# Performance work log

Hardware: AMD Instinct MI355X
Metric: run time of the kernel (lower is better)

The kernel has to match this reference:

```python
import jax, jax.numpy as jnp
import numpy as np

B, T, D, H = 512, 64, 16, 1024  # H must equal T*D (required by the original reshape)


def setup_inputs() -> dict:
    key = jax.random.key(0)
    ks = list(jax.random.split(key, 30))
    def nrm(k, shape, s=0.05):
        return jax.random.normal(k, shape, dtype=jnp.float32) * s
    inp = {}
    inp["values"] = jax.random.normal(ks[0], (B, T, D), dtype=jnp.float32)
    inp["masks"] = (jax.random.uniform(ks[1], (B, T, D)) < 0.8).astype(jnp.float32)
    i = 2
    for pre in ("fw", "bw"):
        for l, din in ((0, D), (1, H)):
            inp[f"{pre}_Wih{l}"] = nrm(ks[i], (4 * H, din)); i += 1
            inp[f"{pre}_Whh{l}"] = nrm(ks[i], (4 * H, H)); i += 1
            inp[f"{pre}_bih{l}"] = nrm(ks[i], (4 * H,)); i += 1
            inp[f"{pre}_bhh{l}"] = nrm(ks[i], (4 * H,)); i += 1
    inp["out_W"] = nrm(ks[i], (D, H)); i += 1
    inp["out_b"] = nrm(ks[i], (D,)); i += 1
    inp["fcb_W"] = nrm(ks[i], (D, 1)); i += 1
    inp["fcb_b"] = nrm(ks[i], (D,)); i += 1
    inp["fce_W"] = nrm(ks[i], (D, 1)); i += 1
    inp["fce_b"] = nrm(ks[i], (D,)); i += 1
    return inp


def _lstm_cell(x, h, c, Wih, Whh, bih, bhh):
    # PyTorch LSTMCell: gate order i, f, g, o
    gates = x @ Wih.T + bih + h @ Whh.T + bhh
    i, f, g, o = jnp.split(gates, 4, axis=-1)
    c2 = jax.nn.sigmoid(f) * c + jax.nn.sigmoid(i) * jnp.tanh(g)
    return jax.nn.sigmoid(o) * jnp.tanh(c2), c2


def _forward(values, masks, fw_Wih0, fw_Whh0, fw_bih0, fw_bhh0, fw_Wih1, fw_Whh1, fw_bih1, fw_bhh1,
             bw_Wih0, bw_Whh0, bw_bih0, bw_bhh0, bw_Wih1, bw_Whh1, bw_bih1, bw_bhh1,
             out_W, out_b, fcb_W, fcb_b, fce_W, fce_b):
    Bc, Tc, Dc = values.shape
    zeros = jnp.zeros((Bc, H), values.dtype)
    bwd_values = jnp.flip(values, 1)
    bwd_masks = jnp.flip(masks, 1)
    # fc_begin/fc_end outputs are dead code in the original (init loop starts at layer 1)
    # Original pre-loop: layers 1..L-1 run once with zero inputs/states.
    hf1, cf1 = _lstm_cell(zeros, zeros, zeros, fw_Wih1, fw_Whh1, fw_bih1, fw_bhh1)
    hb1, cb1 = _lstm_cell(zeros, zeros, zeros, bw_Wih1, bw_Whh1, bw_bih1, bw_bhh1)
    carry0 = (zeros, zeros, hf1, cf1, zeros, zeros, hb1, cb1)

    def step(carry, xs):
        hf0, cf0, hf1, cf1, hb0, cb0, hb1, cb1 = carry
        x_f, m_f, x_b, m_b = xs
        cc_f = (1.0 - m_f) * (hf1 @ out_W.T + out_b) + m_f * x_f
        cc_b = (1.0 - m_b) * (hb1 @ out_W.T + out_b) + m_b * x_b
        hf0, cf0 = _lstm_cell(cc_f, hf0, cf0, fw_Wih0, fw_Whh0, fw_bih0, fw_bhh0)
        hf1, cf1 = _lstm_cell(hf0, hf1, cf1, fw_Wih1, fw_Whh1, fw_bih1, fw_bhh1)
        hb0, cb0 = _lstm_cell(cc_b, hb0, cb0, bw_Wih0, bw_Whh0, bw_bih0, bw_bhh0)
        hb1, cb1 = _lstm_cell(hb0, hb1, cb1, bw_Wih1, bw_Whh1, bw_bih1, bw_bhh1)
        return (hf0, cf0, hf1, cf1, hb0, cb0, hb1, cb1), None

    xs = (jnp.swapaxes(values, 0, 1), jnp.swapaxes(masks, 0, 1),
          jnp.swapaxes(bwd_values, 0, 1), jnp.swapaxes(bwd_masks, 0, 1))
    carry, _ = jax.lax.scan(step, carry0, xs)
    hf1, hb1 = carry[2], carry[6]
    # Original averages fwd with hidden-dim-flipped bwd hidden state
    h = (hf1 + jnp.flip(hb1, 1)) * 0.5
    imputations = h.reshape(Bc, Tc, Dc)
    imputed = imputations * (1.0 - masks) + values * masks
    return h, imputations, imputed


def reference(values, masks, fw_Wih0, fw_Whh0, fw_bih0, fw_bhh0, fw_Wih1, fw_Whh1, fw_bih1, fw_bhh1,
              bw_Wih0, bw_Whh0, bw_bih0, bw_bhh0, bw_Wih1, bw_Whh1, bw_bih1, bw_bhh1,
              out_W, out_b, fcb_W, fcb_b, fce_W, fce_b):
    return _forward(values, masks, fw_Wih0, fw_Whh0, fw_bih0, fw_bhh0, fw_Wih1, fw_Whh1, fw_bih1, fw_bhh1,
                    bw_Wih0, bw_Whh0, bw_bih0, bw_bhh0, bw_Wih1, bw_Whh1, bw_bih1, bw_bhh1,
                    out_W, out_b, fcb_W, fcb_b, fce_W, fce_b)
```

## Files before the change

### kernel.cpp

```cpp
#include <hip/hip_runtime.h>
#include <cstdint>
#include <cstddef>

typedef unsigned short u16;
typedef __attribute__((ext_vector_type(8))) short short8;
typedef __attribute__((ext_vector_type(4))) short short4v;
typedef __attribute__((ext_vector_type(4))) float f32x4;

#define NB 512
#define NT 64
#define ND 16
#define NH 1024
#define LDSBUF 12288

__device__ __forceinline__ u16 f2bf(float x) {
  union { float f; unsigned u; } v; v.f = x;
  unsigned r = v.u + 0x7fffu + ((v.u >> 16) & 1u);
  return (u16)(r >> 16);
}
__device__ __forceinline__ float bf2f(u16 u) {
  union { float f; unsigned u; } v; v.u = ((unsigned)u) << 16;
  return v.f;
}
__device__ __forceinline__ float sigf(float x) { return 1.f / (1.f + __expf(-x)); }

__device__ __forceinline__ void glds16(const void* g, void* l) {
  __builtin_amdgcn_global_load_lds((const __attribute__((address_space(1))) void*)g,
                                   (__attribute__((address_space(3))) void*)l, 16, 0, 0);
}

__device__ __forceinline__ int swz(int row, int col) {
  return ((((col >> 3) ^ (row & 7)) << 3) | (col & 7));
}

__device__ __forceinline__ int inv_np(int np) {
  int hb = np >> 6, g = (np >> 4) & 3, hlo = np & 15;
  return g * 1024 + hb * 16 + hlo;
}

__global__ void k_prep_big(const float* s0, const float* s1, const float* s2,
                           const float* s3, const float* s4, const float* s5, u16* dst) {
  for (unsigned q = blockIdx.x * 256 + threadIdx.x; q < (6u << 20); q += gridDim.x * 256) {
    int mat = q >> 20;
    int rem = q & ((1 << 20) - 1);
    int np = rem >> 8;
    int k = (rem & 255) * 4;
    int row = inv_np(np);
    const float* s = mat == 0 ? s0 : mat == 1 ? s1 : mat == 2 ? s2 : mat == 3 ? s3 : mat == 4 ? s4 : s5;
    float4 v = *(const float4*)(s + (size_t)row * NH + k);
    u16* d = dst + (size_t)mat * 4194304 + (size_t)np * NH + swz(np, k);
    d[0] = f2bf(v.x); d[1] = f2bf(v.y); d[2] = f2bf(v.z); d[3] = f2bf(v.w);
  }
}

__global__ void k_prep_small(const float* fwih0, const float* bwih0,
                             const float* fbi0, const float* fbh0, const float* fbi1, const float* fbh1,
                             const float* bbi0, const float* bbh0, const float* bbi1, const float* bbh1,
                             const float* outW,
                             u16* wih0p, float* biasb, u16* owbf) {
  int idx = blockIdx.x * 256 + threadIdx.x;
  if (idx < 524288) {
    int dir = idx >> 18;
    int r = idx & 262143;
    int np = r >> 6, d = r & 63;
    int row = inv_np(np);
    const float* s = dir ? bwih0 : fwih0;
    float v = (d < 16) ? s[row * 16 + d] : 0.f;
    wih0p[(size_t)dir * 262144 + (size_t)np * 64 + swz(np, d)] = f2bf(v);
  } else if (idx < 524288 + 16384) {
    int j = idx - 524288;
    int which = j >> 12;
    int np = j & 4095;
    int row = inv_np(np);
    const float* bi = which == 0 ? fbi0 : which == 1 ? fbi1 : which == 2 ? bbi0 : bbi1;
    const float* bh = which == 0 ? fbh0 : which == 1 ? fbh1 : which == 2 ? bbh0 : bbh1;
    biasb[which * 4096 + np] = bi[row] + bh[row];
  } else if (idx < 524288 + 16384 + 16384) {
    int j = idx - 524288 - 16384;
    owbf[j] = f2bf(outW[j]);
  }
}

__global__ void k_init(const float* fbi1, const float* fbh1, const float* bbi1, const float* bbh1,
                       float* c0, float* c1, u16* h0bf, u16* h1bf) {
  int idx = blockIdx.x * 256 + threadIdx.x;
  int dir = idx >> 19;
  int rem = idx & ((1 << 19) - 1);
  int b = rem >> 10, h = rem & 1023;
  const float* bi = dir ? bbi1 : fbi1;
  const float* bh = dir ? bbh1 : fbh1;
  float gi = bi[h] + bh[h];
  float gg = bi[2048 + h] + bh[2048 + h];
  float go = bi[3072 + h] + bh[3072 + h];
  float c = sigf(gi) * tanhf(gg);
  float hv = sigf(go) * tanhf(c);
  size_t o = (size_t)dir * 524288 + rem;
  c1[o] = c;
  h1bf[(size_t)(dir * 2) * 524288 + (size_t)b * NH + swz(b, h)] = f2bf(hv);
  c0[o] = 0.f;
  h0bf[(size_t)(dir * 2) * 524288 + rem] = 0;
}

__global__ __launch_bounds__(256) void k_cc0(const u16* h1f, const u16* h1b,
                                             const float* outW, float* partial) {
  int dir = blockIdx.y;
  int w = threadIdx.x >> 6, lane = threadIdx.x & 63;
  int b = blockIdx.x * 4 + w;
  const u16* hb = dir ? h1b : h1f;
  int key = b & 7;
  short8 ha = *(const short8*)(hb + (size_t)b * NH + ((lane * 2) ^ key) * 8);
  short8 hc = *(const short8*)(hb + (size_t)b * NH + ((lane * 2 + 1) ^ key) * 8);
  float hf[16];
#pragma unroll
  for (int j = 0; j < 8; ++j) { hf[j] = bf2f((u16)ha[j]); hf[8 + j] = bf2f((u16)hc[j]); }
  float sums[16];
#pragma unroll
  for (int d = 0; d < 16; ++d) {
    const float* wr = outW + (size_t)d * NH + lane * 16;
    float s = 0.f;
#pragma unroll
    for (int j = 0; j < 16; ++j) s += hf[j] * wr[j];
#pragma unroll
    for (int off = 32; off; off >>= 1) s += __shfl_xor(s, off);
    sums[d] = s;
  }
  if (lane == 0) {
    float* dst = partial + (size_t)dir * 524288 + (size_t)b * 16;
#pragma unroll
    for (int d = 0; d < 16; ++d) dst[d] = sums[d];
  }
}

struct StepCtx {
  u16* h0bf; u16* h1bf;
  const u16* wbig; const u16* wih0p;
  const float* biasb;
  float* c0; float* c1;
  float* partial;
  const float* values; const float* masks; const float* outb;
  const u16* owbf;
};

__device__ __forceinline__ void phase_g0(u16* SM, const StepCtx& a, int dir,
                                         int m_blk, int n_blk, int t, int p) {
  const int m0 = m_blk * 64, n0 = n_blk * 128;
  const int tid = threadIdx.x, w = tid >> 6, lane = tid & 63;
  const int srow = lane >> 3, scol = (lane & 7) * 8;
  const int wm = w >> 1, wn = w & 1;
  const int fr = lane & 15, fq = lane >> 4;
  const int key = fr & 7;
  const u16* h0_in = a.h0bf + (size_t)(dir * 2 + p) * 524288;
  u16* h0_out = a.h0bf + (size_t)(dir * 2 + 1 - p) * 524288;
  const u16* W00 = a.wbig + (size_t)(dir * 3 + 0) * 4194304;
  const u16* Wcc = a.wih0p + (size_t)dir * 262144;
  const float* bias0 = a.biasb + (size_t)dir * 2 * 4096;
  float* cs0 = a.c0 + (size_t)dir * 524288;

  int aoff[2][2], boff[4][2];
#pragma unroll
  for (int mi = 0; mi < 2; ++mi)
#pragma unroll
    for (int kk = 0; kk < 2; ++kk)
      aoff[mi][kk] = (wm * 32 + mi * 16 + fr) * 64 + ((fq + kk * 4) ^ key) * 8;
#pragma unroll
  for (int ni = 0; ni < 4; ++ni)
#pragma unroll
    for (int kk = 0; kk < 2; ++kk)
      boff[ni][kk] = 4096 + (wn * 64 + ni * 16 + fr) * 64 + ((fq + kk * 4) ^ key) * 8;

  f32x4 acc[2][4];
#pragma unroll
  for (int i = 0; i < 2; ++i)
#pragma unroll
    for (int j = 0; j < 4; ++j) acc[i][j] = f32x4{0.f, 0.f, 0.f, 0.f};

  {
    const int rl = tid >> 2, q = tid & 3;
    const int grow = m0 + rl;
    const int d4 = q * 4;
    float4 ps = {0.f, 0.f, 0.f, 0.f};
    const float* pp = a.partial + (size_t)dir * 524288 + (size_t)grow * 16 + d4;
    for (int nb = 0; nb < 64; ++nb) {
      float4 v = *(const float4*)(pp + (size_t)nb * 8192);
      ps.x += v.x; ps.y += v.y; ps.z += v.z; ps.w += v.w;
    }
    int tt = dir ? (NT - 1 - t) : t;
    float4 x = *(const float4*)(a.values + ((size_t)grow * NT + tt) * ND + d4);
    float4 m = *(const float4*)(a.masks + ((size_t)grow * NT + tt) * ND + d4);
    float4 ob = *(const float4*)(a.outb + d4);
    short4v cc;
    cc[0] = (short)f2bf((1.f - m.x) * (ps.x + ob.x) + m.x * x.x);
    cc[1] = (short)f2bf((1.f - m.y) * (ps.y + ob.y) + m.y * x.y);
    cc[2] = (short)f2bf((1.f - m.z) * (ps.z + ob.z) + m.z * x.z);
    cc[3] = (short)f2bf((1.f - m.w) * (ps.w + ob.w) + m.w * x.w);
    int k2 = rl & 7;
    *(short4v*)(SM + rl * 64 + (((d4 >> 3) ^ k2) << 3) + (d4 & 7)) = cc;
    short8 z8 = {0, 0, 0, 0, 0, 0, 0, 0};
    *(short8*)(SM + rl * 64 + (((2 + q) ^ k2) << 3)) = z8;
    if (q < 2) *(short8*)(SM + rl * 64 + (((6 + q) ^ k2) << 3)) = z8;
    asm volatile("s_waitcnt lgkmcnt(0)" ::: "memory");
    __builtin_amdgcn_sched_barrier(0);
  }

  auto stage0 = [&](int c) {
    int buf = c; while (buf >= 3) buf -= 3;
    u16* lb = SM + buf * LDSBUF;
    if (c == 0) {
#pragma unroll
      for (int k = 0; k < 4; ++k)
        glds16(Wcc + (size_t)(n0 + w * 32 + k * 8 + srow) * 64 + scol,
               lb + 4096 + (w * 32 + k * 8) * 64);
      return;
    }
    int ci = c - 1;
    const u16* pa = h0_in + (size_t)ci * 64;
    const u16* pw = W00 + (size_t)ci * 64;
    glds16(pa + (size_t)(m0 + w * 16 + srow) * NH + scol, lb + (w * 16) * 64);
    glds16(pa + (size_t)(m0 + w * 16 + 8 + srow) * NH + scol, lb + (w * 16 + 8) * 64);
#pragma unroll
    for (int k = 0; k < 4; ++k)
      glds16(pw + (size_t)(n0 + w * 32 + k * 8 + srow) * NH + scol,
             lb + 4096 + (w * 32 + k * 8) * 64);
  };

  stage0(0); stage0(1);
  for (int c = 0; c < 17; ++c) {
    if (c == 16) asm volatile("s_waitcnt vmcnt(0)" ::: "memory");
    else         asm volatile("s_waitcnt vmcnt(6)" ::: "memory");
    __builtin_amdgcn_s_barrier();
    __builtin_amdgcn_sched_barrier(0);
    if (c + 2 < 17) stage0(c + 2);
    int buf = c; while (buf >= 3) buf -= 3;
    const u16* base = SM + buf * LDSBUF;
    short8 af[2][2], bb[4][2];
#pragma unroll
    for (int kk = 0; kk < 2; ++kk) {
#pragma unroll
      for (int mi = 0; mi < 2; ++mi) af[mi][kk] = *(const short8*)(base + aoff[mi][kk]);
#pragma unroll
      for (int ni = 0; ni < 4; ++ni) bb[ni][kk] = *(const short8*)(base + boff[ni][kk]);
    }
#pragma unroll
    for (int kk = 0; kk < 2; ++kk)
#pragma unroll
      for (int mi = 0; mi < 2; ++mi)
#pragma unroll
        for (int ni = 0; ni < 4; ++ni)
          acc[mi][ni] = __builtin_amdgcn_mfma_f32_16x16x32_bf16(af[mi][kk], bb[ni][kk], acc[mi][ni], 0, 0, 0);
  }

  const int hg = ((n0 + wn * 64) >> 2) + fr;
  const float b0 = bias0[n0 + wn * 64 + fr];
  const float b1 = bias0[n0 + wn * 64 + 16 + fr];
  const float b2 = bias0[n0 + wn * 64 + 32 + fr];
  const float b3 = bias0[n0 + wn * 64 + 48 + fr];
#pragma unroll
  for (int mi = 0; mi < 2; ++mi)
#pragma unroll
    for (int r = 0; r < 4; ++r) {
      int row = m0 + wm * 32 + mi * 16 + fq * 4 + r;
      size_t sidx = (size_t)row * NH + hg;
      float iv = acc[mi][0][r] + b0;
      float fv = acc[mi][1][r] + b1;
      float gv = acc[mi][2][r] + b2;
      float ov = acc[mi][3][r] + b3;
      float cp = cs0[sidx];
      float c2 = sigf(fv) * cp + sigf(iv) * tanhf(gv);
      float hvv = sigf(ov) * tanhf(c2);
      cs0[sidx] = c2;
      h0_out[(size_t)row * NH + swz(row, hg)] = f2bf(hvv);
    }
}

__device__ __forceinline__ void phase_g1(u16* SM, const StepCtx& a, int dir,
                                         int m_blk, int n_blk, int t, int p) {
  const int m0 = m_blk * 64, n0 = n_blk * 128;
  const int tid = threadIdx.x, w = tid >> 6, lane = tid & 63;
  const int srow = lane >> 3, scol = (lane & 7) * 8;
  const int wm = w >> 1, wn = w & 1;
  const int fr = lane & 15, fq = lane >> 4;
  const int key = fr & 7;
  const u16* h0_new = a.h0bf + (size_t)(dir * 2 + 1 - p) * 524288;
  const u16* h1_in = a.h1bf + (size_t)(dir * 2 + p) * 524288;
  u16* h1_out = a.h1bf + (size_t)(dir * 2 + 1 - p) * 524288;
  const u16* W10 = a.wbig + (size_t)(dir * 3 + 1) * 4194304;
  const u16* W11 = a.wbig + (size_t)(dir * 3 + 2) * 4194304;
  const float* bias1 = a.biasb + (size_t)(dir * 2 + 1) * 4096;
  float* cs1 = a.c1 + (size_t)dir * 524288;

  int aoff[2][2], boff[4][2];
#pragma unroll
  for (int mi = 0; mi < 2; ++mi)
#pragma unroll
    for (int kk = 0; kk < 2; ++kk)
      aoff[mi][kk] = (wm * 32 + mi * 16 + fr) * 64 + ((fq + kk * 4) ^ key) * 8;
#pragma unroll
  for (int ni = 0; ni < 4; ++ni)
#pragma unroll
    for (int kk = 0; kk < 2; ++kk)
      boff[ni][kk] = 4096 + (wn * 64 + ni * 16 + fr) * 64 + ((fq + kk * 4) ^ key) * 8;

  f32x4 acc[2][4];
#pragma unroll
  for (int i = 0; i < 2; ++i)
#pragma unroll
    for (int j = 0; j < 4; ++j) acc[i][j] = f32x4{0.f, 0.f, 0.f, 0.f};

  auto stage1 = [&](int c) {
    int buf = c; while (buf >= 3) buf -= 3;
    u16* lb = SM + buf * LDSBUF;
    const u16* pa; const u16* pw;
    if (c < 16) { pa = h0_new + (size_t)c * 64; pw = W10 + (size_t)c * 64; }
    else { pa = h1_in + (size_t)(c - 16) * 64; pw = W11 + (size_t)(c - 16) * 64; }
    glds16(pa + (size_t)(m0 + w * 16 + srow) * NH + scol, lb + (w * 16) * 64);
    glds16(pa + (size_t)(m0 + w * 16 + 8 + srow) * NH + scol, lb + (w * 16 + 8) * 64);
#pragma unroll
    for (int k = 0; k < 4; ++k)
      glds16(pw + (size_t)(n0 + w * 32 + k * 8 + srow) * NH + scol,
             lb + 4096 + (w * 32 + k * 8) * 64);
  };

  stage1(0); stage1(1);
  for (int c = 0; c < 32; ++c) {
    if (c == 31) asm volatile("s_waitcnt vmcnt(0)" ::: "memory");
    else         asm volatile("s_waitcnt vmcnt(6)" ::: "memory");
    __builtin_amdgcn_s_barrier();
    __builtin_amdgcn_sched_barrier(0);
    if (c + 2 < 32) stage1(c + 2);
    int buf = c; while (buf >= 3) buf -= 3;
    const u16* base = SM + buf * LDSBUF;
    short8 af[2][2], bb[4][2];
#pragma unroll
    for (int kk = 0; kk < 2; ++kk) {
#pragma unroll
      for (int mi = 0; mi < 2; ++mi) af[mi][kk] = *(const short8*)(base + aoff[mi][kk]);
#pragma unroll
      for (int ni = 0; ni < 4; ++ni) bb[ni][kk] = *(const short8*)(base + boff[ni][kk]);
    }
#pragma unroll
    for (int kk = 0; kk < 2; ++kk)
#pragma unroll
      for (int mi = 0; mi < 2; ++mi)
#pragma unroll
        for (int ni = 0; ni < 4; ++ni)
          acc[mi][ni] = __builtin_amdgcn_mfma_f32_16x16x32_bf16(af[mi][kk], bb[ni][kk], acc[mi][ni], 0, 0, 0);
  }

  const int hb4 = (n0 + wn * 64) >> 2;
  const int hg = hb4 + fr;
  const float b0 = bias1[n0 + wn * 64 + fr];
  const float b1 = bias1[n0 + wn * 64 + 16 + fr];
  const float b2 = bias1[n0 + wn * 64 + 32 + fr];
  const float b3 = bias1[n0 + wn * 64 + 48 + fr];
  float hsv[2][4];
#pragma unroll
  for (int mi = 0; mi < 2; ++mi)
#pragma unroll
    for (int r = 0; r < 4; ++r) {
      int row = m0 + wm * 32 + mi * 16 + fq * 4 + r;
      size_t sidx = (size_t)row * NH + hg;
      float iv = acc[mi][0][r] + b0;
      float fv = acc[mi][1][r] + b1;
      float gv = acc[mi][2][r] + b2;
      float ov = acc[mi][3][r] + b3;
      float cp = cs1[sidx];
      float c2 = sigf(fv) * cp + sigf(iv) * tanhf(gv);
      float hvv = sigf(ov) * tanhf(c2);
      cs1[sidx] = c2;
      h1_out[(size_t)row * NH + swz(row, hg)] = f2bf(hvv);
      hsv[mi][r] = hvv;
    }

  {
    u16* ts = SM + w * 512;
    *(short4v*)(ts + (lane >> 2) * 32 + 16 + (lane & 3) * 4) = short4v{0, 0, 0, 0};
    short8 afr = {0, 0, 0, 0, 0, 0, 0, 0};
    if (fq < 2) afr = *(const short8*)(a.owbf + (size_t)fr * NH + hb4 + fq * 8);
    float* pout = a.partial + ((size_t)(dir * 64 + n_blk * 2 + wn) * 512) * 16;
#pragma unroll
    for (int mi = 0; mi < 2; ++mi) {
#pragma unroll
      for (int r = 0; r < 4; ++r)
        *(ts + (fq * 4 + r) * 32 + fr) = f2bf(hsv[mi][r]);
      asm volatile("s_waitcnt lgkmcnt(0)" ::: "memory");
      __builtin_amdgcn_sched_barrier(0);
      short8 bfr2 = *(const short8*)(ts + fr * 32 + fq * 8);
      f32x4 pz = {0.f, 0.f, 0.f, 0.f};
      pz = __builtin_amdgcn_mfma_f32_16x16x32_bf16(afr, bfr2, pz, 0, 0, 0);
      int row = m0 + wm * 32 + mi * 16 + fr;
      float4 st = {pz[0], pz[1], pz[2], pz[3]};
      *(float4*)(pout + (size_t)row * 16 + fq * 4) = st;
      asm volatile("s_waitcnt lgkmcnt(0)" ::: "memory");
      __builtin_amdgcn_sched_barrier(0);
    }
  }
}

__global__ __launch_bounds__(256) void k_g0(StepCtx a, int t) {
  __shared__ u16 SM[3 * LDSBUF];
  phase_g0(SM, a, blockIdx.z, blockIdx.y, blockIdx.x, t, t & 1);
}
__global__ __launch_bounds__(256) void k_g1(StepCtx a, int t) {
  __shared__ u16 SM[3 * LDSBUF];
  phase_g1(SM, a, blockIdx.z, blockIdx.y, blockIdx.x, t, t & 1);
}

__global__ void k_final(const u16* hf1, const u16* hb1, const float* values,
                        const float* masks, float* out) {
  int idx = blockIdx.x * 256 + threadIdx.x;
  int b = idx >> 10, j = idx & 1023;
  float hf = bf2f(hf1[(size_t)b * NH + swz(b, j)]);
  int jr = NH - 1 - j;
  float hb = bf2f(hb1[(size_t)b * NH + swz(b, jr)]);
  float hv = 0.5f * (hf + hb);
  float m = masks[idx];
  out[idx] = hv;
  out[524288 + idx] = hv;
  out[1048576 + idx] = hv * (1.f - m) + values[idx] * m;
}

extern "C" void kernel_launch(void* const* d_in, const int* in_sizes, int n_in,
                              void* d_out, int out_size, void* d_ws, size_t ws_size,
                              hipStream_t stream) {
  const float* values  = (const float*)d_in[0];
  const float* masks   = (const float*)d_in[1];
  const float* fw_Wih0 = (const float*)d_in[2];
  const float* fw_Whh0 = (const float*)d_in[3];
  const float* fw_bih0 = (const float*)d_in[4];
  const float* fw_bhh0 = (const float*)d_in[5];
  const float* fw_Wih1 = (const float*)d_in[6];
  const float* fw_Whh1 = (const float*)d_in[7];
  const float* fw_bih1 = (const float*)d_in[8];
  const float* fw_bhh1 = (const float*)d_in[9];
  const float* bw_Wih0 = (const float*)d_in[10];
  const float* bw_Whh0 = (const float*)d_in[11];
  const float* bw_bih0 = (const float*)d_in[12];
  const float* bw_bhh0 = (const float*)d_in[13];
  const float* bw_Wih1 = (const float*)d_in[14];
  const float* bw_Whh1 = (const float*)d_in[15];
  const float* bw_bih1 = (const float*)d_in[16];
  const float* bw_bhh1 = (const float*)d_in[17];
  const float* out_W   = (const float*)d_in[18];
  const float* out_b   = (const float*)d_in[19];

  char* ws = (char*)d_ws;
  u16* wbig    = (u16*)ws;
  u16* wih0p   = (u16*)(ws + 50331648);
  float* biasb = (float*)(ws + 51380224);
  u16* owbf    = (u16*)(ws + 51445760);
  float* c0    = (float*)(ws + 51478528);
  float* c1    = (float*)(ws + 55672832);
  u16* h0bf    = (u16*)(ws + 59867136);
  u16* h1bf    = (u16*)(ws + 64061440);
  float* partial = (float*)(ws + 68255744);
  if (ws_size < 72450048) return;

  k_prep_big<<<4096, 256, 0, stream>>>(fw_Whh0, fw_Wih1, fw_Whh1, bw_Whh0, bw_Wih1, bw_Whh1, wbig);
  k_prep_small<<<2176, 256, 0, stream>>>(fw_Wih0, bw_Wih0, fw_bih0, fw_bhh0, fw_bih1, fw_bhh1,
                                         bw_bih0, bw_bhh0, bw_bih1, bw_bhh1, out_W,
                                         wih0p, biasb, owbf);
  k_init<<<4096, 256, 0, stream>>>(fw_bih1, fw_bhh1, bw_bih1, bw_bhh1, c0, c1, h0bf, h1bf);
  hipMemsetAsync(partial, 0, 4194304, stream);
  k_cc0<<<dim3(128, 2), 256, 0, stream>>>(h1bf, h1bf + (size_t)2 * 524288, out_W, partial);

  StepCtx sc;
  sc.h0bf = h0bf; sc.h1bf = h1bf;
  sc.wbig = wbig; sc.wih0p = wih0p;
  sc.biasb = biasb; sc.c0 = c0; sc.c1 = c1;
  sc.partial = partial;
  sc.values = values; sc.masks = masks; sc.outb = out_b;
  sc.owbf = owbf;

  for (int t = 0; t < NT; ++t) {
    k_g0<<<dim3(32, 8, 2), 256, 0, stream>>>(sc, t);
    k_g1<<<dim3(32, 8, 2), 256, 0, stream>>>(sc, t);
  }

  k_final<<<2048, 256, 0, stream>>>(h1bf, h1bf + (size_t)2 * 524288, values, masks, (float*)d_out);
}
```

Measured before the change: 3.178 ms.

## Load MFMA fragments directly from global memory with prepacked weight layout

The recurrent GEMM kernels stop staging A and B tiles through LDS with async global-to-LDS copies and barriers. Instead, weights are repacked at prep time into an MFMA-fragment-major layout so each lane reads its short8 fragment straight from global memory into registers, and the h activations are read directly with the matching swizzled offsets. Fragments are double-buffered in registers, and LDS shrinks to a small buffer used only for the input-concat tile. This removes LDS traffic and per-chunk barriers and raises potential occupancy, at the cost of more register pressure and no LDS-level sharing of tiles across the waves in a block (each A/B fragment is now fetched per wave from global/L2).

```diff
diff --git a/kernel.cpp b/kernel.cpp
--- a/kernel.cpp
+++ b/kernel.cpp
@@ -11,7 +11,6 @@
 #define NT 64
 #define ND 16
 #define NH 1024
-#define LDSBUF 12288
 
 __device__ __forceinline__ u16 f2bf(float x) {
   union { float f; unsigned u; } v; v.f = x;
@@ -23,11 +22,6 @@
   return v.f;
 }
 __device__ __forceinline__ float sigf(float x) { return 1.f / (1.f + __expf(-x)); }
-
-__device__ __forceinline__ void glds16(const void* g, void* l) {
-  __builtin_amdgcn_global_load_lds((const __attribute__((address_space(1))) void*)g,
-                                   (__attribute__((address_space(3))) void*)l, 16, 0, 0);
-}
 
 __device__ __forceinline__ int swz(int row, int col) {
   return ((((col >> 3) ^ (row & 7)) << 3) | (col & 7));
@@ -48,7 +42,8 @@
     int row = inv_np(np);
     const float* s = mat == 0 ? s0 : mat == 1 ? s1 : mat == 2 ? s2 : mat == 3 ? s3 : mat == 4 ? s4 : s5;
     float4 v = *(const float4*)(s + (size_t)row * NH + k);
-    u16* d = dst + (size_t)mat * 4194304 + (size_t)np * NH + swz(np, k);
+    int nb = np >> 4, fr = np & 15, kb = k >> 5, fq = (k >> 3) & 3, e = k & 7;
+    u16* d = dst + (size_t)mat * 4194304 + (size_t)((nb * 32 + kb) * 64 + fq * 16 + fr) * 8 + e;
     d[0] = f2bf(v.x); d[1] = f2bf(v.y); d[2] = f2bf(v.z); d[3] = f2bf(v.w);
   }
 }
@@ -66,7 +61,8 @@
     int row = inv_np(np);
     const float* s = dir ? bwih0 : fwih0;
     float v = (d < 16) ? s[row * 16 + d] : 0.f;
-    wih0p[(size_t)dir * 262144 + (size_t)np * 64 + swz(np, d)] = f2bf(v);
+    int nb = np >> 4, fr = np & 15, kb = d >> 5, fq = (d >> 3) & 3, e = d & 7;
+    wih0p[(size_t)dir * 262144 + (size_t)((nb * 2 + kb) * 64 + fq * 16 + fr) * 8 + e] = f2bf(v);
   } else if (idx < 524288 + 16384) {
     int j = idx - 524288;
     int which = j >> 12;
@@ -131,6 +127,19 @@
   }
 }
 
+struct Frags { short8 a[4]; short8 b[8]; };
+
+__device__ __forceinline__ void domfma(const Frags& F, f32x4 (&acc)[2][4]) {
+#pragma unroll
+  for (int kk = 0; kk < 2; ++kk)
+#pragma unroll
+    for (int mi = 0; mi < 2; ++mi)
+#pragma unroll
+      for (int ni = 0; ni < 4; ++ni)
+        acc[mi][ni] = __builtin_amdgcn_mfma_f32_16x16x32_bf16(F.a[mi * 2 + kk], F.b[ni * 2 + kk],
+                                                              acc[mi][ni], 0, 0, 0);
+}
+
 struct StepCtx {
   u16* h0bf; u16* h1bf;
   const u16* wbig; const u16* wih0p;
@@ -145,34 +154,48 @@
                                          int m_blk, int n_blk, int t, int p) {
   const int m0 = m_blk * 64, n0 = n_blk * 128;
   const int tid = threadIdx.x, w = tid >> 6, lane = tid & 63;
-  const int srow = lane >> 3, scol = (lane & 7) * 8;
   const int wm = w >> 1, wn = w & 1;
-  const int fr = lane & 15, fq = lane >> 4;
-  const int key = fr & 7;
+  const int fr = lane & 15, fq = lane >> 4, key = fr & 7;
+  const int lane8 = lane * 8;
+  const int nbb = n_blk * 8 + wn * 4;
   const u16* h0_in = a.h0bf + (size_t)(dir * 2 + p) * 524288;
   u16* h0_out = a.h0bf + (size_t)(dir * 2 + 1 - p) * 524288;
   const u16* W00 = a.wbig + (size_t)(dir * 3 + 0) * 4194304;
   const u16* Wcc = a.wih0p + (size_t)dir * 262144;
   const float* bias0 = a.biasb + (size_t)dir * 2 * 4096;
   float* cs0 = a.c0 + (size_t)dir * 524288;
-
-  int aoff[2][2], boff[4][2];
+  const u16* hA = h0_in + (size_t)m0 * NH;
+
+  int voffA[4];
 #pragma unroll
   for (int mi = 0; mi < 2; ++mi)
 #pragma unroll
     for (int kk = 0; kk < 2; ++kk)
-      aoff[mi][kk] = (wm * 32 + mi * 16 + fr) * 64 + ((fq + kk * 4) ^ key) * 8;
+      voffA[mi * 2 + kk] = (wm * 32 + mi * 16 + fr) * NH + ((fq + kk * 4) ^ key) * 8;
+
+  f32x4 acc[2][4];
+#pragma unroll
+  for (int i = 0; i < 2; ++i)
+#pragma unroll
+    for (int j = 0; j < 4; ++j) acc[i][j] = f32x4{0.f, 0.f, 0.f, 0.f};
+
+  Frags f0, fA, fB;
 #pragma unroll
   for (int ni = 0; ni < 4; ++ni)
 #pragma unroll
     for (int kk = 0; kk < 2; ++kk)
-      boff[ni][kk] = 4096 + (wn * 64 + ni * 16 + fr) * 64 + ((fq + kk * 4) ^ key) * 8;
-
-  f32x4 acc[2][4];
-#pragma unroll
-  for (int i = 0; i < 2; ++i)
-#pragma unroll
-    for (int j = 0; j < 4; ++j) acc[i][j] = f32x4{0.f, 0.f, 0.f, 0.f};
+      f0.b[ni * 2 + kk] = *(const short8*)(Wcc + (size_t)((nbb + ni) * 2 + kk) * 512 + lane8);
+  auto LD0 = [&](int c, Frags& F) {
+    int ci = c - 1;
+#pragma unroll
+    for (int i = 0; i < 4; ++i) F.a[i] = *(const short8*)(hA + ci * 64 + voffA[i]);
+#pragma unroll
+    for (int ni = 0; ni < 4; ++ni)
+#pragma unroll
+      for (int kk = 0; kk < 2; ++kk)
+        F.b[ni * 2 + kk] = *(const short8*)(W00 + (size_t)((nbb + ni) * 32 + ci * 2 + kk) * 512 + lane8);
+  };
+  LD0(1, fA); LD0(2, fB);
 
   {
     const int rl = tid >> 2, q = tid & 3;
@@ -201,52 +224,19 @@
     asm volatile("s_waitcnt lgkmcnt(0)" ::: "memory");
     __builtin_amdgcn_sched_barrier(0);
   }
-
-  auto stage0 = [&](int c) {
-    int buf = c; while (buf >= 3) buf -= 3;
-    u16* lb = SM + buf * LDSBUF;
-    if (c == 0) {
-#pragma unroll
-      for (int k = 0; k < 4; ++k)
-        glds16(Wcc + (size_t)(n0 + w * 32 + k * 8 + srow) * 64 + scol,
-               lb + 4096 + (w * 32 + k * 8) * 64);
-      return;
-    }
-    int ci = c - 1;
-    const u16* pa = h0_in + (size_t)ci * 64;
-    const u16* pw = W00 + (size_t)ci * 64;
-    glds16(pa + (size_t)(m0 + w * 16 + srow) * NH + scol, lb + (w * 16) * 64);
-    glds16(pa + (size_t)(m0 + w * 16 + 8 + srow) * NH + scol, lb + (w * 16 + 8) * 64);
-#pragma unroll
-    for (int k = 0; k < 4; ++k)
-      glds16(pw + (size_t)(n0 + w * 32 + k * 8 + srow) * NH + scol,
-             lb + 4096 + (w * 32 + k * 8) * 64);
-  };
-
-  stage0(0); stage0(1);
-  for (int c = 0; c < 17; ++c) {
-    if (c == 16) asm volatile("s_waitcnt vmcnt(0)" ::: "memory");
-    else         asm volatile("s_waitcnt vmcnt(6)" ::: "memory");
-    __builtin_amdgcn_s_barrier();
-    __builtin_amdgcn_sched_barrier(0);
-    if (c + 2 < 17) stage0(c + 2);
-    int buf = c; while (buf >= 3) buf -= 3;
-    const u16* base = SM + buf * LDSBUF;
-    short8 af[2][2], bb[4][2];
-#pragma unroll
-    for (int kk = 0; kk < 2; ++kk) {
-#pragma unroll
-      for (int mi = 0; mi < 2; ++mi) af[mi][kk] = *(const short8*)(base + aoff[mi][kk]);
-#pragma unroll
-      for (int ni = 0; ni < 4; ++ni) bb[ni][kk] = *(const short8*)(base + boff[ni][kk]);
-    }
+  __builtin_amdgcn_s_barrier();
+
+#pragma unroll
+  for (int mi = 0; mi < 2; ++mi)
 #pragma unroll
     for (int kk = 0; kk < 2; ++kk)
-#pragma unroll
-      for (int mi = 0; mi < 2; ++mi)
-#pragma unroll
-        for (int ni = 0; ni < 4; ++ni)
-          acc[mi][ni] = __builtin_amdgcn_mfma_f32_16x16x32_bf16(af[mi][kk], bb[ni][kk], acc[mi][ni], 0, 0, 0);
+      f0.a[mi * 2 + kk] = *(const short8*)(SM + (wm * 32 + mi * 16 + fr) * 64 + ((fq + kk * 4) ^ key) * 8);
+  domfma(f0, acc);
+  for (int c = 1; c < 17; c += 2) {
+    domfma(fA, acc);
+    if (c + 2 < 17) LD0(c + 2, fA);
+    domfma(fB, acc);
+    if (c + 3 < 17) LD0(c + 3, fB);
   }
 
   const int hg = ((n0 + wn * 64) >> 2) + fr;
@@ -276,10 +266,10 @@
                                          int m_blk, int n_blk, int t, int p) {
   const int m0 = m_blk * 64, n0 = n_blk * 128;
   const int tid = threadIdx.x, w = tid >> 6, lane = tid & 63;
-  const int srow = lane >> 3, scol = (lane & 7) * 8;
   const int wm = w >> 1, wn = w & 1;
-  const int fr = lane & 15, fq = lane >> 4;
-  const int key = fr & 7;
+  const int fr = lane & 15, fq = lane >> 4, key = fr & 7;
+  const int lane8 = lane * 8;
+  const int nbb = n_blk * 8 + wn * 4;
   const u16* h0_new = a.h0bf + (size_t)(dir * 2 + 1 - p) * 524288;
   const u16* h1_in = a.h1bf + (size_t)(dir * 2 + p) * 524288;
   u16* h1_out = a.h1bf + (size_t)(dir * 2 + 1 - p) * 524288;
@@ -287,18 +277,15 @@
   const u16* W11 = a.wbig + (size_t)(dir * 3 + 2) * 4194304;
   const float* bias1 = a.biasb + (size_t)(dir * 2 + 1) * 4096;
   float* cs1 = a.c1 + (size_t)dir * 524288;
-
-  int aoff[2][2], boff[4][2];
+  const u16* hA0 = h0_new + (size_t)m0 * NH;
+  const u16* hA1 = h1_in + (size_t)m0 * NH;
+
+  int voffA[4];
 #pragma unroll
   for (int mi = 0; mi < 2; ++mi)
 #pragma unroll
     for (int kk = 0; kk < 2; ++kk)
-      aoff[mi][kk] = (wm * 32 + mi * 16 + fr) * 64 + ((fq + kk * 4) ^ key) * 8;
-#pragma unroll
-  for (int ni = 0; ni < 4; ++ni)
-#pragma unroll
-    for (int kk = 0; kk < 2; ++kk)
-      boff[ni][kk] = 4096 + (wn * 64 + ni * 16 + fr) * 64 + ((fq + kk * 4) ^ key) * 8;
+      voffA[mi * 2 + kk] = (wm * 32 + mi * 16 + fr) * NH + ((fq + kk * 4) ^ key) * 8;
 
   f32x4 acc[2][4];
 #pragma unroll
@@ -306,44 +293,26 @@
 #pragma unroll
     for (int j = 0; j < 4; ++j) acc[i][j] = f32x4{0.f, 0.f, 0.f, 0.f};
 
-  auto stage1 = [&](int c) {
-    int buf = c; while (buf >= 3) buf -= 3;
-    u16* lb = SM + buf * LDSBUF;
-    const u16* pa; const u16* pw;
-    if (c < 16) { pa = h0_new + (size_t)c * 64; pw = W10 + (size_t)c * 64; }
-    else { pa = h1_in + (size_t)(c - 16) * 64; pw = W11 + (size_t)(c - 16) * 64; }
-    glds16(pa + (size_t)(m0 + w * 16 + srow) * NH + scol, lb + (w * 16) * 64);
-    glds16(pa + (size_t)(m0 + w * 16 + 8 + srow) * NH + scol, lb + (w * 16 + 8) * 64);
-#pragma unroll
-    for (int k = 0; k < 4; ++k)
-      glds16(pw + (size_t)(n0 + w * 32 + k * 8 + srow) * NH + scol,
-             lb + 4096 + (w * 32 + k * 8) * 64);
+  auto LD1 = [&](int c, Frags& F) {
+    const u16* ha = (c < 16) ? hA0 : hA1;
+    const u16* wb = (c < 16) ? W10 : W11;
+    int ci = (c < 16) ? c : c - 16;
+#pragma unroll
+    for (int i = 0; i < 4; ++i) F.a[i] = *(const short8*)(ha + ci * 64 + voffA[i]);
+#pragma unroll
+    for (int ni = 0; ni < 4; ++ni)
+#pragma unroll
+      for (int kk = 0; kk < 2; ++kk)
+        F.b[ni * 2 + kk] = *(const short8*)(wb + (size_t)((nbb + ni) * 32 + ci * 2 + kk) * 512 + lane8);
   };
 
-  stage1(0); stage1(1);
-  for (int c = 0; c < 32; ++c) {
-    if (c == 31) asm volatile("s_waitcnt vmcnt(0)" ::: "memory");
-    else         asm volatile("s_waitcnt vmcnt(6)" ::: "memory");
-    __builtin_amdgcn_s_barrier();
-    __builtin_amdgcn_sched_barrier(0);
-    if (c + 2 < 32) stage1(c + 2);
-    int buf = c; while (buf >= 3) buf -= 3;
-    const u16* base = SM + buf * LDSBUF;
-    short8 af[2][2], bb[4][2];
-#pragma unroll
-    for (int kk = 0; kk < 2; ++kk) {
-#pragma unroll
-      for (int mi = 0; mi < 2; ++mi) af[mi][kk] = *(const short8*)(base + aoff[mi][kk]);
-#pragma unroll
-      for (int ni = 0; ni < 4; ++ni) bb[ni][kk] = *(const short8*)(base + boff[ni][kk]);
-    }
-#pragma unroll
-    for (int kk = 0; kk < 2; ++kk)
-#pragma unroll
-      for (int mi = 0; mi < 2; ++mi)
-#pragma unroll
-        for (int ni = 0; ni < 4; ++ni)
-          acc[mi][ni] = __builtin_amdgcn_mfma_f32_16x16x32_bf16(af[mi][kk], bb[ni][kk], acc[mi][ni], 0, 0, 0);
+  Frags fA, fB;
+  LD1(0, fA); LD1(1, fB);
+  for (int c = 0; c < 32; c += 2) {
+    domfma(fA, acc);
+    if (c + 2 < 32) LD1(c + 2, fA);
+    domfma(fB, acc);
+    if (c + 3 < 32) LD1(c + 3, fB);
   }
 
   const int hb4 = (n0 + wn * 64) >> 2;
@@ -397,11 +366,11 @@
 }
 
 __global__ __launch_bounds__(256) void k_g0(StepCtx a, int t) {
-  __shared__ u16 SM[3 * LDSBUF];
+  __shared__ u16 SM[4096];
   phase_g0(SM, a, blockIdx.z, blockIdx.y, blockIdx.x, t, t & 1);
 }
 __global__ __launch_bounds__(256) void k_g1(StepCtx a, int t) {
-  __shared__ u16 SM[3 * LDSBUF];
+  __shared__ u16 SM[4096];
   phase_g1(SM, a, blockIdx.z, blockIdx.y, blockIdx.x, t, t & 1);
 }
 
```

New measurement: 3.781 ms. +19.0%, slower.
